# Kernel tuning notes

Hardware: AMD Instinct MI355X
Metric: run time of the kernel (lower is better)

## Reference

```python
import jax, jax.numpy as jnp
import numpy as np

H = 1024

def setup_inputs() -> dict:
    key = jax.random.key(0)
    k1, k2, k3, k4 = jax.random.split(key, 4)
    hidden = jax.random.normal(k1, (1, 64, H), dtype=jnp.float32)
    encoder_outputs = jax.random.normal(k2, (2048, 64, H), dtype=jnp.float32)
    # nn.Linear(H, H) params: weight [out,in], bias [out]
    W = jax.random.normal(k3, (H, H), dtype=jnp.float32) * (1.0 / np.sqrt(H))
    b = jax.random.normal(k4, (H,), dtype=jnp.float32) * 0.01
    return {"hidden": hidden, "encoder_outputs": encoder_outputs, "W": W, "b": b}

def reference(hidden, encoder_outputs, W, b):
    # method == 'general': energy[l,b] = hidden[0,b] . (W @ enc[l,b] + bias)
    # enc: [L, B, H]; projected: [L, B, H]
    proj = jnp.einsum('lbh,kh->lbk', encoder_outputs, W) + b
    # attn_energies: [B, L]
    attn_energies = jnp.einsum('bh,lbh->bl', hidden[0], proj)
    # faithful to F.softmax(..., dim=0): softmax over the BATCH axis
    attn = jax.nn.softmax(attn_energies, axis=0)
    return attn[:, None, :]  # [B, 1, L]
```

## Files before the change

kernel.cpp:

```cpp
#include <hip/hip_runtime.h>
#include <hip/hip_bf16.h>

#define H 1024
#define B 64
#define KC 8
#define KLEN (H / KC)
#define LT 2

typedef float floatx4 __attribute__((ext_vector_type(4)));

__global__ __launch_bounds__(256) void projA1(
    const float* __restrict__ hidden,
    const float* __restrict__ W,
    float* __restrict__ part)
{
    const int b0 = blockIdx.x * 2;
    const int kc = blockIdx.y;
    const int t  = threadIdx.x;
    const float* h0 = hidden + (size_t)b0 * H + (size_t)kc * KLEN;
    const float* h1 = h0 + H;
    const float4* Wr = (const float4*)(W + (size_t)kc * KLEN * H) + t;

    float4 a0 = {0.f, 0.f, 0.f, 0.f};
    float4 a1 = {0.f, 0.f, 0.f, 0.f};
    #pragma unroll 8
    for (int k = 0; k < KLEN; ++k) {
        const float4 w = Wr[(size_t)k * (H / 4)];
        const float s0 = h0[k];
        const float s1 = h1[k];
        a0.x += s0 * w.x; a0.y += s0 * w.y; a0.z += s0 * w.z; a0.w += s0 * w.w;
        a1.x += s1 * w.x; a1.y += s1 * w.y; a1.z += s1 * w.z; a1.w += s1 * w.w;
    }
    ((float4*)(part + ((size_t)kc * B + b0) * H))[t]     = a0;
    ((float4*)(part + ((size_t)kc * B + b0 + 1) * H))[t] = a1;
}

__global__ __launch_bounds__(256) void projA2(
    const float* __restrict__ part,
    const float* __restrict__ hidden,
    const float* __restrict__ bias,
    float* __restrict__ u,
    float* __restrict__ c)
{
    const int b = blockIdx.x;
    const int t = threadIdx.x;

    float4 a = {0.f, 0.f, 0.f, 0.f};
    #pragma unroll
    for (int kc = 0; kc < KC; ++kc) {
        const float4 p = ((const float4*)(part + ((size_t)kc * B + b) * H))[t];
        a.x += p.x; a.y += p.y; a.z += p.z; a.w += p.w;
    }
    ((float4*)(u + (size_t)b * H))[t] = a;

    float s = 0.f;
    #pragma unroll
    for (int j = 0; j < H / 256; ++j)
        s += hidden[(size_t)b * H + t + j * 256] * bias[t + j * 256];
    __shared__ float red[256];
    red[t] = s;
    __syncthreads();
    for (int st = 128; st > 0; st >>= 1) {
        if (t < st) red[t] += red[t + st];
        __syncthreads();
    }
    if (t == 0) c[b] = red[0];
}

__global__ __launch_bounds__(256) void energy_softmax_fused(
    const float* __restrict__ enc,
    const float* __restrict__ u,
    const float* __restrict__ c,
    float* __restrict__ out,
    int L)
{
    const int l0   = blockIdx.x * LT;
    const int wave = threadIdx.x >> 6;
    const int lane = threadIdx.x & 63;

    __shared__ float e_s[LT][B];

    #pragma unroll
    for (int i = 0; i < LT; ++i) {
        const int l = l0 + i;
        const float* encl = enc + (size_t)l * B * H;
        #pragma unroll 4
        for (int j = 0; j < 16; ++j) {
            const int b = wave * 16 + j;
            const floatx4* e4 = (const floatx4*)(encl + (size_t)b * H);
            const float4*  u4 = (const float4*)(u + (size_t)b * H);
            float acc = 0.f;
            #pragma unroll
            for (int q = 0; q < 4; ++q) {
                const floatx4 v  = __builtin_nontemporal_load(e4 + lane + q * 64);
                const float4  uu = u4[lane + q * 64];
                acc += v.x * uu.x + v.y * uu.y + v.z * uu.z + v.w * uu.w;
            }
            #pragma unroll
            for (int off = 32; off > 0; off >>= 1) acc += __shfl_down(acc, off, 64);
            if (lane == 0) e_s[i][b] = acc + c[b];
        }
    }
    __syncthreads();

    if (wave < LT) {
        const float e = e_s[wave][lane];
        float m = e;
        #pragma unroll
        for (int off = 32; off > 0; off >>= 1) m = fmaxf(m, __shfl_xor(m, off, 64));
        const float ex = __expf(e - m);
        float s = ex;
        #pragma unroll
        for (int off = 32; off > 0; off >>= 1) s += __shfl_xor(s, off, 64);
        out[(size_t)lane * L + l0 + wave] = ex / s;
    }
}

extern "C" void kernel_launch(void* const* d_in, const int* in_sizes, int n_in,
                              void* d_out, int out_size, void* d_ws, size_t ws_size,
                              hipStream_t stream) {
    const float* hidden = (const float*)d_in[0];
    const float* enc    = (const float*)d_in[1];
    const float* W      = (const float*)d_in[2];
    const float* bias   = (const float*)d_in[3];
    float* out = (float*)d_out;

    const int L = in_sizes[1] / (B * H);

    float* part = (float*)d_ws;
    float* u    = part + (size_t)KC * B * H;
    float* c    = u + (size_t)B * H;

    dim3 gridA1(B / 2, KC);
    projA1<<<gridA1, 256, 0, stream>>>(hidden, W, part);

    projA2<<<B, 256, 0, stream>>>(part, hidden, bias, u, c);

    energy_softmax_fused<<<L / LT, 256, 0, stream>>>(enc, u, c, out, L);
}
```

Before: 117.0 us.

## Reuse u across four sequence positions and coalesce softmax output writes

The energy kernel now handles four sequence positions per block and swaps its loops so each wave loads its u row and bias term once, then reuses them across all four positions. The softmax results are staged in shared memory and written out with four consecutive positions per batch row instead of one scattered store per lane. The projection kernel also computes four batch rows per block so each W load is reused more. This cuts redundant u traffic, but it halves the number of blocks in both kernels and adds a second barrier.

```diff
diff --git a/kernel.cpp b/kernel.cpp
--- a/kernel.cpp
+++ b/kernel.cpp
@@ -5,7 +5,7 @@
 #define B 64
 #define KC 8
 #define KLEN (H / KC)
-#define LT 2
+#define LT 4
 
 typedef float floatx4 __attribute__((ext_vector_type(4)));
 
@@ -14,25 +14,32 @@
     const float* __restrict__ W,
     float* __restrict__ part)
 {
-    const int b0 = blockIdx.x * 2;
+    const int b0 = blockIdx.x * 4;
     const int kc = blockIdx.y;
     const int t  = threadIdx.x;
-    const float* h0 = hidden + (size_t)b0 * H + (size_t)kc * KLEN;
+    const float* h0 = hidden + (size_t)(b0 + 0) * H + (size_t)kc * KLEN;
     const float* h1 = h0 + H;
+    const float* h2 = h1 + H;
+    const float* h3 = h2 + H;
     const float4* Wr = (const float4*)(W + (size_t)kc * KLEN * H) + t;
 
     float4 a0 = {0.f, 0.f, 0.f, 0.f};
     float4 a1 = {0.f, 0.f, 0.f, 0.f};
+    float4 a2 = {0.f, 0.f, 0.f, 0.f};
+    float4 a3 = {0.f, 0.f, 0.f, 0.f};
     #pragma unroll 8
     for (int k = 0; k < KLEN; ++k) {
         const float4 w = Wr[(size_t)k * (H / 4)];
-        const float s0 = h0[k];
-        const float s1 = h1[k];
+        const float s0 = h0[k], s1 = h1[k], s2 = h2[k], s3 = h3[k];
         a0.x += s0 * w.x; a0.y += s0 * w.y; a0.z += s0 * w.z; a0.w += s0 * w.w;
         a1.x += s1 * w.x; a1.y += s1 * w.y; a1.z += s1 * w.z; a1.w += s1 * w.w;
+        a2.x += s2 * w.x; a2.y += s2 * w.y; a2.z += s2 * w.z; a2.w += s2 * w.w;
+        a3.x += s3 * w.x; a3.y += s3 * w.y; a3.z += s3 * w.z; a3.w += s3 * w.w;
     }
-    ((float4*)(part + ((size_t)kc * B + b0) * H))[t]     = a0;
+    ((float4*)(part + ((size_t)kc * B + b0 + 0) * H))[t] = a0;
     ((float4*)(part + ((size_t)kc * B + b0 + 1) * H))[t] = a1;
+    ((float4*)(part + ((size_t)kc * B + b0 + 2) * H))[t] = a2;
+    ((float4*)(part + ((size_t)kc * B + b0 + 3) * H))[t] = a3;
 }
 
 __global__ __launch_bounds__(256) void projA2(
@@ -80,30 +87,32 @@
 
     __shared__ float e_s[LT][B];
 
-    #pragma unroll
-    for (int i = 0; i < LT; ++i) {
-        const int l = l0 + i;
-        const float* encl = enc + (size_t)l * B * H;
-        #pragma unroll 4
-        for (int j = 0; j < 16; ++j) {
-            const int b = wave * 16 + j;
-            const floatx4* e4 = (const floatx4*)(encl + (size_t)b * H);
-            const float4*  u4 = (const float4*)(u + (size_t)b * H);
+    for (int j = 0; j < 16; ++j) {
+        const int b = wave * 16 + j;
+        const float4* u4 = (const float4*)(u + (size_t)b * H);
+        float4 uu[4];
+        #pragma unroll
+        for (int q = 0; q < 4; ++q) uu[q] = u4[lane + q * 64];
+        const float cb = c[b];
+
+        #pragma unroll
+        for (int i = 0; i < LT; ++i) {
+            const int l = l0 + i;
+            const floatx4* e4 = (const floatx4*)(enc + ((size_t)l * B + b) * H);
             float acc = 0.f;
             #pragma unroll
             for (int q = 0; q < 4; ++q) {
-                const floatx4 v  = __builtin_nontemporal_load(e4 + lane + q * 64);
-                const float4  uu = u4[lane + q * 64];
-                acc += v.x * uu.x + v.y * uu.y + v.z * uu.z + v.w * uu.w;
+                const floatx4 v = __builtin_nontemporal_load(e4 + lane + q * 64);
+                acc += v.x * uu[q].x + v.y * uu[q].y + v.z * uu[q].z + v.w * uu[q].w;
             }
             #pragma unroll
             for (int off = 32; off > 0; off >>= 1) acc += __shfl_down(acc, off, 64);
-            if (lane == 0) e_s[i][b] = acc + c[b];
+            if (lane == 0) e_s[i][b] = acc + cb;
         }
     }
     __syncthreads();
 
-    if (wave < LT) {
+    {
         const float e = e_s[wave][lane];
         float m = e;
         #pragma unroll
@@ -112,7 +121,14 @@
         float s = ex;
         #pragma unroll
         for (int off = 32; off > 0; off >>= 1) s += __shfl_xor(s, off, 64);
-        out[(size_t)lane * L + l0 + wave] = ex / s;
+        e_s[wave][lane] = ex / s;
+    }
+    __syncthreads();
+
+    {
+        const int b  = threadIdx.x >> 2;
+        const int li = threadIdx.x & 3;
+        out[(size_t)b * L + l0 + li] = e_s[li][b];
     }
 }
 
@@ -131,7 +147,7 @@
     float* u    = part + (size_t)KC * B * H;
     float* c    = u + (size_t)B * H;
 
-    dim3 gridA1(B / 2, KC);
+    dim3 gridA1(B / 4, KC);
     projA1<<<gridA1, 256, 0, stream>>>(hidden, W, part);
 
     projA2<<<B, 256, 0, stream>>>(part, hidden, bias, u, c);
```

Result: faster. 98.31 us (median of 2 runs) (-16.0%).
